# Optimization experiments

Hardware: AMD Instinct MI355X
Metric: run time of the kernel (lower is better)

## Reference

```python
import jax, jax.numpy as jnp
import numpy as np

NX = NY = 128
N = NX * NY            # 16384 tiles
F = 26                 # in_feats
H = 512                # hidden_dim
NH = 8                 # heads
HD = H // NH           # head_dim = 64
DEPTH = 4
LN_EPS = 1e-5


def _grid_edge_index(nx, ny):
    """4-connected grid, bidirectional edges (src, dst) like _build_grid_edge_index."""
    idx = np.arange(nx * ny).reshape(nx, ny)
    hs, hd = idx[:, :-1].ravel(), idx[:, 1:].ravel()   # horizontal neighbors
    vs, vd = idx[:-1, :].ravel(), idx[1:, :].ravel()   # vertical neighbors
    src = np.concatenate([hs, hd, vs, vd]).astype(np.int32)
    dst = np.concatenate([hd, hs, vd, vs]).astype(np.int32)
    return src, dst


def setup_inputs() -> dict:
    key = jax.random.key(0)
    ks = jax.random.split(key, 8)
    s = 0.02
    src, dst = _grid_edge_index(NX, NY)
    return {
        "graph": jax.random.normal(ks[0], (N, F), jnp.float32),
        "edge_src": jnp.asarray(src),
        "edge_dst": jnp.asarray(dst),
        "Wp": jax.random.normal(ks[1], (F, H), jnp.float32) * s,
        "bp": jnp.zeros((H,), jnp.float32),
        "Wq": jax.random.normal(ks[2], (DEPTH, H, H), jnp.float32) * s,
        "bq": jnp.zeros((DEPTH, H), jnp.float32),
        "Wk": jax.random.normal(ks[3], (DEPTH, H, H), jnp.float32) * s,
        "bk": jnp.zeros((DEPTH, H), jnp.float32),
        "Wv": jax.random.normal(ks[4], (DEPTH, H, H), jnp.float32) * s,
        "bv": jnpp_zeros((DEPTH, H)) if False else jnp.zeros((DEPTH, H), jnp.float32),
        "Ws": jax.random.normal(ks[5], (DEPTH, H, H), jnp.float32) * s,
        "bs": jnp.zeros((DEPTH, H), jnp.float32),
        "Wbeta": jax.random.normal(ks[6], (DEPTH, 3 * H), jnp.float32) * s,
        "ln_g": jnp.ones((DEPTH, H), jnp.float32),
        "ln_b": jnp.zeros((DEPTH, H), jnp.float32),
    }


def _layernorm(x, g, b):
    mu = x.mean(-1, keepdims=True)
    var = ((x - mu) ** 2).mean(-1, keepdims=True)
    return (x - mu) * jax.lax.rsqrt(var + LN_EPS) * g + b


def _transformer_conv(x, src, dst, Wq, bq, Wk, bk, Wv, bv, Ws, bs, Wbeta):
    n = x.shape[0]
    q = (x @ Wq + bq).reshape(n, NH, HD)
    k = (x @ Wk + bk).reshape(n, NH, HD)
    v = (x @ Wv + bv).reshape(n, NH, HD)
    # per-edge attention logits: query at target (dst), key at source (src)
    alpha = (q[dst] * k[src]).sum(-1) / jnp.sqrt(jnp.float32(HD))  # (E, NH)
    # segment softmax over incoming edges of each target node (PyG softmax)
    m = jax.ops.segment_max(alpha, dst, num_segments=n)
    e = jnp.exp(alpha - m[dst])
    denom = jax.ops.segment_sum(e, dst, num_segments=n)
    a = e / (denom[dst] + 1e-16)
    # beta-gated scatter-add aggregation
    out = jax.ops.segment_sum(a[:, :, None] * v[src], dst, num_segments=n)
    out = out.reshape(n, H)
    r = x @ Ws + bs                                  # root/skip projection
    g = jax.nn.sigmoid(jnp.concatenate([out, r, out - r], -1) @ Wbeta)  # (n,)
    g = g[:, None]
    return g * r + (1.0 - g) * out


def reference(graph, edge_src, edge_dst, Wp, bp, Wq, bq, Wk, bk, Wv, bv,
              Ws, bs, Wbeta, ln_g, ln_b):
    x = graph @ Wp + bp
    for l in range(DEPTH):
        h = _transformer_conv(x, edge_src, edge_dst, Wq[l], bq[l], Wk[l], bk[l],
                              Wv[l], bv[l], Ws[l], bs[l], Wbeta[l])
        x = _layernorm(x + h, ln_g[l], ln_b[l])
    global_emb = x.mean(0, keepdims=True)
    return (x, global_emb)


def jnp_zeros(shape):  # unused helper guard
    return jnp.zeros(shape, jnp.float32)

jnp_p_zeros = None

def jnp_zeros_unused():
    pass

# fix accidental typo-safe alias used in setup_inputs
jnp_zeros_f = jnp.zeros

def jnp_noop():
    pass

jnp_zeros2 = jnp.zeros

def jnp_p_zeros_fn(shape):
    return jnp.zeros(shape, jnp.float32)

jnp_p_zeros = jnp_p_zeros_fn

def jnp_zeros3(shape):
    return jnp.zeros(shape, jnp.float32)

jnp_p = jnp

def jnp_zeros4(shape):
    return jnp.zeros(shape, jnp.float32)

jnp_zeros5 = jnp.zeros

def jnp_zeros6(shape):
    return jnp.zeros(shape, jnp.float32)

jnp_p_zeros_alias = jnp.zeros

def jnp_p_zeros_(shape):
    return jnp.zeros(shape, jnp.float32)

jnp_p_zeros__ = jnp.zeros

# alias referenced defensively inside setup_inputs (never called)
jnp_p_zeros___ = jnp.zeros

def jnp_p_zeros____(shape):
    return jnp.zeros(shape, jnp.float32)

jnp_p_zeros_____ = jnp.zeros

jnp_p_zeros______ = jnp.zeros

jnp_p_zeros_______ = jnp.zeros

jnp_p_zeros________ = jnp.zeros

jnp_p_zeros_________ = jnp.zeros

jnp_p_zeros__________ = jnp.zeros

# name used in the dead branch of setup_inputs
jnp_p_zeros = jnp.zeros

def jnp_p_zeros_def(shape):
    return jnp.zeros(shape, jnp.float32)

jnpp_zeros = jnp.zeros
```

## Files before the change

### kernel.cpp

```cpp
#include <hip/hip_runtime.h>
#include <hip/hip_bf16.h>
#include <math.h>

#define NN    16384
#define FF    26
#define HH    512
#define NHEAD 8
#define HDIM  64
#define GRID_W 128
#define LN_EPS 1e-5f

typedef __attribute__((ext_vector_type(8))) short short8;
typedef __attribute__((ext_vector_type(4))) float f32x4;
typedef __attribute__((ext_vector_type(4))) short s16x4;

static __device__ __forceinline__ float bf2f(short u) {
  unsigned int x = ((unsigned int)(unsigned short)u) << 16;
  return __uint_as_float(x);
}
static __device__ __forceinline__ short f2bf(float f) {
  __hip_bfloat16 h = __float2bfloat16(f);
  return __builtin_bit_cast(short, h);
}

__global__ __launch_bounds__(256) void wconv_kernel(
    const float* __restrict__ Wq, const float* __restrict__ Wk,
    const float* __restrict__ Wv, const float* __restrict__ Ws,
    __hip_bfloat16* __restrict__ Wt) {
  __shared__ float ls[32][33];
  int bid = blockIdx.x;
  int mi = bid >> 8, kt = (bid >> 4) & 15, nt = bid & 15;
  int l = mi >> 2, m = mi & 3;
  const float* src = ((m == 0) ? Wq : (m == 1) ? Wk : (m == 2) ? Wv : Ws)
                   + (size_t)l * 262144;
  int c = threadIdx.x & 31, r = threadIdx.x >> 5;
#pragma unroll
  for (int p = 0; p < 4; ++p)
    ls[r + 8 * p][c] = src[(size_t)(kt * 32 + r + 8 * p) * 512 + nt * 32 + c];
  __syncthreads();
#pragma unroll
  for (int p = 0; p < 4; ++p)
    Wt[((size_t)mi * 512 + nt * 32 + r + 8 * p) * 512 + kt * 32 + c] =
        __float2bfloat16(ls[c][r + 8 * p]);
}

__global__ __launch_bounds__(256) void prep_kernel(
    const float* __restrict__ graph, const float* __restrict__ Wp,
    const float* __restrict__ bq, const float* __restrict__ bk,
    const float* __restrict__ bv, const float* __restrict__ bs,
    __hip_bfloat16* __restrict__ gb, __hip_bfloat16* __restrict__ Wpt,
    float* __restrict__ bcat) {
  int b = blockIdx.x;
  if (b < 2048) {
    int tid = b * 256 + threadIdx.x;
    int n = tid >> 5, k = tid & 31;
    gb[tid] = __float2bfloat16(k < FF ? graph[n * FF + k] : 0.f);
  } else if (b < 2112) {
    int tid = (b - 2048) * 256 + threadIdx.x;
    int j = tid >> 5, k = tid & 31;
    Wpt[tid] = __float2bfloat16(k < FF ? Wp[k * HH + j] : 0.f);
  } else {
    int tid = (b - 2112) * 256 + threadIdx.x;
    int j = tid & 511;
    int m = (tid >> 9) & 3;
    int l = tid >> 11;
    const float* src = (m == 0) ? bq : (m == 1) ? bk : (m == 2) ? bv : bs;
    bcat[tid] = src[l * 512 + j];
  }
}

template <int LDA, int KDIM, int LDC, bool WF32>
__global__ __launch_bounds__(256) void gemm_t(
    const __hip_bfloat16* __restrict__ A,
    const __hip_bfloat16* __restrict__ Bt,
    const float* __restrict__ bias,
    __hip_bfloat16* __restrict__ C,
    float* __restrict__ Xf) {
  __shared__ __align__(16) char lds[16384];
  const int t    = threadIdx.x;
  const int wv   = t >> 6;
  const int lane = t & 63;
  const int m0 = blockIdx.x * 128, n0 = blockIdx.y * 128;

  const int srow = (wv << 4) + (lane >> 2);
  const int gch  = (lane & 3) ^ ((lane >> 3) & 3);
  const char* agp = (const char*)(A  + (size_t)(m0 + srow) * LDA + (gch << 3));
  const char* bgp = (const char*)(Bt + (size_t)(n0 + srow) * KDIM + (gch << 3));
  char* aldst = lds +        (wv << 10) + (lane << 4);
  char* bldst = lds + 8192 + (wv << 10) + (lane << 4);

  const int q  = lane >> 4;
  const int r  = lane & 15;
  const int fs = (r >> 1) & 3;
  const int ksl = ((q ^ fs) << 4);
  const int wm = wv >> 1, wn = wv & 1;
  int aoff[4], boff[4];
#pragma unroll
  for (int i = 0; i < 4; ++i) {
    aoff[i] = (((wm << 6) + (i << 4) + r) << 6) + ksl;
    boff[i] = 8192 + (((wn << 6) + (i << 4) + r) << 6) + ksl;
  }

  f32x4 acc[4][4];
#pragma unroll
  for (int i = 0; i < 4; ++i)
#pragma unroll
    for (int j = 0; j < 4; ++j) acc[i][j] = (f32x4){0.f, 0.f, 0.f, 0.f};

  for (int k0 = 0; k0 < KDIM; k0 += 32) {
    __syncthreads();
    const size_t kb = (size_t)k0 * 2;
    __builtin_amdgcn_global_load_lds(
        (const __attribute__((address_space(1))) void*)(agp + kb),
        (__attribute__((address_space(3))) void*)(aldst), 16, 0, 0);
    __builtin_amdgcn_global_load_lds(
        (const __attribute__((address_space(1))) void*)(agp + kb + (size_t)LDA * 128),
        (__attribute__((address_space(3))) void*)(aldst + 4096), 16, 0, 0);
    __builtin_amdgcn_global_load_lds(
        (const __attribute__((address_space(1))) void*)(bgp + kb),
        (__attribute__((address_space(3))) void*)(bldst), 16, 0, 0);
    __builtin_amdgcn_global_load_lds(
        (const __attribute__((address_space(1))) void*)(bgp + kb + (size_t)KDIM * 128),
        (__attribute__((address_space(3))) void*)(bldst + 4096), 16, 0, 0);
    __syncthreads();

    short8 af[4], bfr[4];
#pragma unroll
    for (int i = 0; i < 4; ++i) af[i]  = *(const short8*)(lds + aoff[i]);
#pragma unroll
    for (int i = 0; i < 4; ++i) bfr[i] = *(const short8*)(lds + boff[i]);
#pragma unroll
    for (int mi = 0; mi < 4; ++mi)
#pragma unroll
      for (int ni = 0; ni < 4; ++ni)
        acc[mi][ni] = __builtin_amdgcn_mfma_f32_16x16x32_bf16(
            af[mi], bfr[ni], acc[mi][ni], 0, 0, 0);
  }

  float bbv[4];
#pragma unroll
  for (int ni = 0; ni < 4; ++ni) bbv[ni] = bias[n0 + (wn << 6) + (ni << 4) + r];

  __syncthreads();

  short* lp = (short*)(lds + (wv << 12));
  const int rl = lane >> 2, sg = lane & 3;
#pragma unroll
  for (int mi = 0; mi < 4; ++mi) {
#pragma unroll
    for (int ni = 0; ni < 4; ++ni)
#pragma unroll
      for (int e = 0; e < 4; ++e)
        lp[((q << 2) + e) * 66 + (ni << 4) + r] = f2bf(acc[mi][ni][e] + bbv[ni]);
    const short* rp = lp + rl * 66 + (sg << 4);
    short8 v0 = *(const short8*)rp;
    short8 v1 = *(const short8*)(rp + 8);
    const int grow = m0 + (wm << 6) + (mi << 4) + rl;
    short8* cp = (short8*)(C + (size_t)grow * LDC + n0 + (wn << 6) + (sg << 4));
    cp[0] = v0;
    cp[1] = v1;
    if (WF32) {
#pragma unroll
      for (int ni = 0; ni < 4; ++ni) {
        const int col = n0 + (wn << 6) + (ni << 4) + r;
        const size_t rb = (size_t)(m0 + (wm << 6) + (mi << 4) + (q << 2));
#pragma unroll
        for (int e = 0; e < 4; ++e)
          Xf[(rb + e) * LDC + col] = acc[mi][ni][e] + bbv[ni];
      }
    }
  }
}

__global__ __launch_bounds__(256) void node_kernel(
    const __hip_bfloat16* __restrict__ qkvs,
    float* __restrict__ x, __hip_bfloat16* __restrict__ xb,
    const float* __restrict__ Wb, const float* __restrict__ lng,
    const float* __restrict__ lnb) {
  const int t = threadIdx.x;
  const int p  = t >> 5;
  const int sl = t & 31;
  const int bi = blockIdx.x;
  const int gi = ((bi >> 5) << 1) + (p >> 2);
  const int gj = ((bi & 31) << 2) + (p & 3);
  const int n = (gi << 7) + gj;

  int nbr[4];
  nbr[0] = (gj > 0)          ? n - 1      : -1;
  nbr[1] = (gj < GRID_W - 1) ? n + 1      : -1;
  nbr[2] = (gi > 0)          ? n - GRID_W : -1;
  nbr[3] = (gi < GRID_W - 1) ? n + GRID_W : -1;

  const int c0 = sl << 4;

  short8 q8a = *(const short8*)(qkvs + (size_t)n * 2048 + c0);
  short8 q8b = *(const short8*)(qkvs + (size_t)n * 2048 + c0 + 8);
  float al[4];
#pragma unroll
  for (int e = 0; e < 4; ++e) {
    const int me = (nbr[e] >= 0) ? nbr[e] : n;
    short8 k8a = *(const short8*)(qkvs + (size_t)me * 2048 + 512 + c0);
    short8 k8b = *(const short8*)(qkvs + (size_t)me * 2048 + 512 + c0 + 8);
    float pp = 0.f;
#pragma unroll
    for (int j = 0; j < 8; ++j)
      pp += bf2f(q8a[j]) * bf2f(k8a[j]) + bf2f(q8b[j]) * bf2f(k8b[j]);
    pp += __shfl_xor(pp, 1);
    pp += __shfl_xor(pp, 2);
    al[e] = (nbr[e] >= 0) ? pp * 0.125f : -1e30f;
  }
  float mx = fmaxf(fmaxf(al[0], al[1]), fmaxf(al[2], al[3]));
  float aw[4], sum = 1e-16f;
#pragma unroll
  for (int e = 0; e < 4; ++e) {
    aw[e] = (nbr[e] >= 0) ? expf(al[e] - mx) : 0.f;
    sum += aw[e];
  }
  float inv = 1.f / sum;
#pragma unroll
  for (int e = 0; e < 4; ++e) aw[e] *= inv;

  float ov[16] = {};
#pragma unroll
  for (int e = 0; e < 4; ++e) {
    if (nbr[e] >= 0) {
      short8 v8a = *(const short8*)(qkvs + (size_t)nbr[e] * 2048 + 1024 + c0);
      short8 v8b = *(const short8*)(qkvs + (size_t)nbr[e] * 2048 + 1024 + c0 + 8);
#pragma unroll
      for (int j = 0; j < 8; ++j) {
        ov[j]     += aw[e] * bf2f(v8a[j]);
        ov[j + 8] += aw[e] * bf2f(v8b[j]);
      }
    }
  }
  short8 s8a = *(const short8*)(qkvs + (size_t)n * 2048 + 1536 + c0);
  short8 s8b = *(const short8*)(qkvs + (size_t)n * 2048 + 1536 + c0 + 8);
  float rv[16];
#pragma unroll
  for (int j = 0; j < 8; ++j) { rv[j] = bf2f(s8a[j]); rv[j + 8] = bf2f(s8b[j]); }

  float part = 0.f;
#pragma unroll
  for (int c = 0; c < 4; ++c) {
    float4 w0 = *(const float4*)(Wb + c0 + c * 4);
    float4 w1 = *(const float4*)(Wb + 512 + c0 + c * 4);
    float4 w2 = *(const float4*)(Wb + 1024 + c0 + c * 4);
    part += ov[c*4+0] * w0.x + ov[c*4+1] * w0.y + ov[c*4+2] * w0.z + ov[c*4+3] * w0.w
          + rv[c*4+0] * w1.x + rv[c*4+1] * w1.y + rv[c*4+2] * w1.z + rv[c*4+3] * w1.w
          + (ov[c*4+0] - rv[c*4+0]) * w2.x + (ov[c*4+1] - rv[c*4+1]) * w2.y
          + (ov[c*4+2] - rv[c*4+2]) * w2.z + (ov[c*4+3] - rv[c*4+3]) * w2.w;
  }
#pragma unroll
  for (int s = 16; s > 0; s >>= 1) part += __shfl_xor(part, s);
  float g = 1.f / (1.f + expf(-part));

  const float4* xp = (const float4*)(x + (size_t)n * HH + c0);
  float y[16], s1 = 0.f, sq = 0.f;
#pragma unroll
  for (int c = 0; c < 4; ++c) {
    float4 xv = xp[c];
    float xa[4] = {xv.x, xv.y, xv.z, xv.w};
#pragma unroll
    for (int u = 0; u < 4; ++u) {
      int j = c * 4 + u;
      y[j] = xa[u] + g * rv[j] + (1.f - g) * ov[j];
      s1 += y[j];
      sq += y[j] * y[j];
    }
  }
#pragma unroll
  for (int s = 16; s > 0; s >>= 1) {
    s1 += __shfl_xor(s1, s);
    sq += __shfl_xor(sq, s);
  }
  float mu  = s1 * (1.f / 512.f);
  float var = sq * (1.f / 512.f) - mu * mu;
  float rs  = rsqrtf(var + LN_EPS);

  float4* xo = (float4*)(x + (size_t)n * HH + c0);
  short8 ob0, ob1;
#pragma unroll
  for (int c = 0; c < 4; ++c) {
    float4 gv = *(const float4*)(lng + c0 + c * 4);
    float4 bv = *(const float4*)(lnb + c0 + c * 4);
    float o0 = (y[c*4+0] - mu) * rs * gv.x + bv.x;
    float o1 = (y[c*4+1] - mu) * rs * gv.y + bv.y;
    float o2 = (y[c*4+2] - mu) * rs * gv.z + bv.z;
    float o3 = (y[c*4+3] - mu) * rs * gv.w + bv.w;
    xo[c] = make_float4(o0, o1, o2, o3);
    if (c < 2) {
      ob0[c*4+0] = f2bf(o0); ob0[c*4+1] = f2bf(o1);
      ob0[c*4+2] = f2bf(o2); ob0[c*4+3] = f2bf(o3);
    } else {
      ob1[(c-2)*4+0] = f2bf(o0); ob1[(c-2)*4+1] = f2bf(o1);
      ob1[(c-2)*4+2] = f2bf(o2); ob1[(c-2)*4+3] = f2bf(o3);
    }
  }
  *(short8*)(xb + (size_t)n * HH + c0) = ob0;
  *(short8*)(xb + (size_t)n * HH + c0 + 8) = ob1;
}

__global__ void zero_kernel(float* __restrict__ p) { p[threadIdx.x] = 0.f; }

__global__ __launch_bounds__(512) void col_mean_kernel(
    const float* __restrict__ x, float* __restrict__ g) {
  int t  = threadIdx.x;
  int n0 = blockIdx.x * 256;
  float s = 0.f;
  for (int rr = 0; rr < 256; ++rr) s += x[(size_t)(n0 + rr) * HH + t];
  atomicAdd(&g[t], s * (1.f / 16384.f));
}

extern "C" void kernel_launch(void* const* d_in, const int* in_sizes, int n_in,
                              void* d_out, int out_size, void* d_ws, size_t ws_size,
                              hipStream_t stream) {
  const float* graph = (const float*)d_in[0];
  const float* Wp = (const float*)d_in[3];
  const float* bp = (const float*)d_in[4];
  const float* Wq = (const float*)d_in[5];
  const float* bq = (const float*)d_in[6];
  const float* Wk = (const float*)d_in[7];
  const float* bk = (const float*)d_in[8];
  const float* Wv = (const float*)d_in[9];
  const float* bv = (const float*)d_in[10];
  const float* Wst = (const float*)d_in[11];
  const float* bst = (const float*)d_in[12];
  const float* Wbeta = (const float*)d_in[13];
  const float* lng = (const float*)d_in[14];
  const float* lnb = (const float*)d_in[15];

  float* x = (float*)d_out;
  char* ws = (char*)d_ws;
  __hip_bfloat16* qkvs = (__hip_bfloat16*)ws;
  __hip_bfloat16* xb   = (__hip_bfloat16*)(ws + 67108864);
  __hip_bfloat16* Wt   = (__hip_bfloat16*)(ws + 83886080);
  __hip_bfloat16* gb   = (__hip_bfloat16*)(ws + 92274688);
  __hip_bfloat16* Wpt  = (__hip_bfloat16*)(ws + 93323264);
  float* bcat          = (float*)(ws + 93356032);

  wconv_kernel<<<4096, 256, 0, stream>>>(Wq, Wk, Wv, Wst, Wt);
  prep_kernel<<<2144, 256, 0, stream>>>(graph, Wp, bq, bk, bv, bst,
                                        gb, Wpt, bcat);

  gemm_t<32, 32, 512, true><<<dim3(128, 4), 256, 0, stream>>>(
      gb, Wpt, bp, xb, x);

  for (int l = 0; l < 4; ++l) {
    gemm_t<512, 512, 2048, false><<<dim3(128, 16), 256, 0, stream>>>(
        xb, Wt + (size_t)l * 4 * 262144, bcat + l * 2048, qkvs, nullptr);
    node_kernel<<<2048, 256, 0, stream>>>(qkvs, x, xb,
        Wbeta + (size_t)l * 1536, lng + (size_t)l * 512, lnb + (size_t)l * 512);
  }

  zero_kernel<<<1, 512, 0, stream>>>(x + (size_t)NN * HH);
  col_mean_kernel<<<64, 512, 0, stream>>>(x, x + (size_t)NN * HH);
}
```

Measured before the change: 443.2 us.

## Switch GEMM to 32x32 MFMA and keep residual stream in bf16 only

The GEMM now uses 32x32x16 bf16 MFMA tiles with direct global stores instead of 16x16x32 MFMAs plus an LDS-staged epilogue. The fp32 copy of the residual stream x is no longer written by the projection GEMM or read and written in the intermediate node layers. The residual is read from the bf16 buffer, and fp32 x is written only in the last layer. This cuts fp32 traffic and removes the LDS epilogue, but the residual now accumulates in bf16, which loses precision, and the epilogue stores are scattered 2-byte writes.

```diff
diff --git a/kernel.cpp b/kernel.cpp
--- a/kernel.cpp
+++ b/kernel.cpp
@@ -10,9 +10,8 @@
 #define GRID_W 128
 #define LN_EPS 1e-5f
 
-typedef __attribute__((ext_vector_type(8))) short short8;
-typedef __attribute__((ext_vector_type(4))) float f32x4;
-typedef __attribute__((ext_vector_type(4))) short s16x4;
+typedef __attribute__((ext_vector_type(8)))  short short8;
+typedef __attribute__((ext_vector_type(16))) float f32x16;
 
 static __device__ __forceinline__ float bf2f(short u) {
   unsigned int x = ((unsigned int)(unsigned short)u) << 16;
@@ -69,13 +68,12 @@
   }
 }
 
-template <int LDA, int KDIM, int LDC, bool WF32>
+template <int LDA, int KDIM, int LDC>
 __global__ __launch_bounds__(256) void gemm_t(
     const __hip_bfloat16* __restrict__ A,
     const __hip_bfloat16* __restrict__ Bt,
     const float* __restrict__ bias,
-    __hip_bfloat16* __restrict__ C,
-    float* __restrict__ Xf) {
+    __hip_bfloat16* __restrict__ C) {
   __shared__ __align__(16) char lds[16384];
   const int t    = threadIdx.x;
   const int wv   = t >> 6;
@@ -89,23 +87,27 @@
   char* aldst = lds +        (wv << 10) + (lane << 4);
   char* bldst = lds + 8192 + (wv << 10) + (lane << 4);
 
-  const int q  = lane >> 4;
-  const int r  = lane & 15;
-  const int fs = (r >> 1) & 3;
-  const int ksl = ((q ^ fs) << 4);
+  const int rr  = lane & 31;
+  const int kg  = lane >> 5;
+  const int fs2 = (rr >> 1) & 3;
   const int wm = wv >> 1, wn = wv & 1;
-  int aoff[4], boff[4];
-#pragma unroll
-  for (int i = 0; i < 4; ++i) {
-    aoff[i] = (((wm << 6) + (i << 4) + r) << 6) + ksl;
-    boff[i] = 8192 + (((wn << 6) + (i << 4) + r) << 6) + ksl;
-  }
-
-  f32x4 acc[4][4];
-#pragma unroll
-  for (int i = 0; i < 4; ++i)
-#pragma unroll
-    for (int j = 0; j < 4; ++j) acc[i][j] = (f32x4){0.f, 0.f, 0.f, 0.f};
+  int aoff[2][2], boff[2][2];
+#pragma unroll
+  for (int ks = 0; ks < 2; ++ks)
+#pragma unroll
+    for (int i = 0; i < 2; ++i) {
+      const int slot = (kg + (ks << 1)) ^ fs2;
+      aoff[ks][i] =        ((((wm << 6) + (i << 5) + rr) << 6) + (slot << 4));
+      boff[ks][i] = 8192 + ((((wn << 6) + (i << 5) + rr) << 6) + (slot << 4));
+    }
+
+  f32x16 acc[2][2];
+#pragma unroll
+  for (int i = 0; i < 2; ++i)
+#pragma unroll
+    for (int j = 0; j < 2; ++j)
+#pragma unroll
+      for (int e = 0; e < 16; ++e) acc[i][j][e] = 0.f;
 
   for (int k0 = 0; k0 < KDIM; k0 += 32) {
     __syncthreads();
@@ -124,57 +126,44 @@
         (__attribute__((address_space(3))) void*)(bldst + 4096), 16, 0, 0);
     __syncthreads();
 
-    short8 af[4], bfr[4];
-#pragma unroll
-    for (int i = 0; i < 4; ++i) af[i]  = *(const short8*)(lds + aoff[i]);
-#pragma unroll
-    for (int i = 0; i < 4; ++i) bfr[i] = *(const short8*)(lds + boff[i]);
-#pragma unroll
-    for (int mi = 0; mi < 4; ++mi)
-#pragma unroll
-      for (int ni = 0; ni < 4; ++ni)
-        acc[mi][ni] = __builtin_amdgcn_mfma_f32_16x16x32_bf16(
-            af[mi], bfr[ni], acc[mi][ni], 0, 0, 0);
-  }
-
-  float bbv[4];
-#pragma unroll
-  for (int ni = 0; ni < 4; ++ni) bbv[ni] = bias[n0 + (wn << 6) + (ni << 4) + r];
-
-  __syncthreads();
-
-  short* lp = (short*)(lds + (wv << 12));
-  const int rl = lane >> 2, sg = lane & 3;
-#pragma unroll
-  for (int mi = 0; mi < 4; ++mi) {
-#pragma unroll
-    for (int ni = 0; ni < 4; ++ni)
-#pragma unroll
-      for (int e = 0; e < 4; ++e)
-        lp[((q << 2) + e) * 66 + (ni << 4) + r] = f2bf(acc[mi][ni][e] + bbv[ni]);
-    const short* rp = lp + rl * 66 + (sg << 4);
-    short8 v0 = *(const short8*)rp;
-    short8 v1 = *(const short8*)(rp + 8);
-    const int grow = m0 + (wm << 6) + (mi << 4) + rl;
-    short8* cp = (short8*)(C + (size_t)grow * LDC + n0 + (wn << 6) + (sg << 4));
-    cp[0] = v0;
-    cp[1] = v1;
-    if (WF32) {
-#pragma unroll
-      for (int ni = 0; ni < 4; ++ni) {
-        const int col = n0 + (wn << 6) + (ni << 4) + r;
-        const size_t rb = (size_t)(m0 + (wm << 6) + (mi << 4) + (q << 2));
-#pragma unroll
-        for (int e = 0; e < 4; ++e)
-          Xf[(rb + e) * LDC + col] = acc[mi][ni][e] + bbv[ni];
+    short8 af[2][2], bfr[2][2];
+#pragma unroll
+    for (int ks = 0; ks < 2; ++ks)
+#pragma unroll
+      for (int i = 0; i < 2; ++i) {
+        af[ks][i]  = *(const short8*)(lds + aoff[ks][i]);
+        bfr[ks][i] = *(const short8*)(lds + boff[ks][i]);
       }
-    }
-  }
-}
-
+#pragma unroll
+    for (int ks = 0; ks < 2; ++ks)
+#pragma unroll
+      for (int mb = 0; mb < 2; ++mb)
+#pragma unroll
+        for (int nb = 0; nb < 2; ++nb)
+          acc[mb][nb] = __builtin_amdgcn_mfma_f32_32x32x16_bf16(
+              af[ks][mb], bfr[ks][nb], acc[mb][nb], 0, 0, 0);
+  }
+
+#pragma unroll
+  for (int nb = 0; nb < 2; ++nb) {
+    const int col = n0 + (wn << 6) + (nb << 5) + rr;
+    const float bb = bias[col];
+#pragma unroll
+    for (int mb = 0; mb < 2; ++mb) {
+      const int rbase = m0 + (wm << 6) + (mb << 5) + (kg << 2);
+#pragma unroll
+      for (int rg = 0; rg < 16; ++rg) {
+        const int row = rbase + (rg & 3) + ((rg >> 2) << 3);
+        C[(size_t)row * LDC + col] = __float2bfloat16(acc[mb][nb][rg] + bb);
+      }
+    }
+  }
+}
+
+template <bool LAST>
 __global__ __launch_bounds__(256) void node_kernel(
     const __hip_bfloat16* __restrict__ qkvs,
-    float* __restrict__ x, __hip_bfloat16* __restrict__ xb,
+    __hip_bfloat16* __restrict__ xb, float* __restrict__ x,
     const float* __restrict__ Wb, const float* __restrict__ lng,
     const float* __restrict__ lnb) {
   const int t = threadIdx.x;
@@ -254,20 +243,16 @@
   for (int s = 16; s > 0; s >>= 1) part += __shfl_xor(part, s);
   float g = 1.f / (1.f + expf(-part));
 
-  const float4* xp = (const float4*)(x + (size_t)n * HH + c0);
+  short8 xr0 = *(const short8*)(xb + (size_t)n * HH + c0);
+  short8 xr1 = *(const short8*)(xb + (size_t)n * HH + c0 + 8);
   float y[16], s1 = 0.f, sq = 0.f;
 #pragma unroll
-  for (int c = 0; c < 4; ++c) {
-    float4 xv = xp[c];
-    float xa[4] = {xv.x, xv.y, xv.z, xv.w};
-#pragma unroll
-    for (int u = 0; u < 4; ++u) {
-      int j = c * 4 + u;
-      y[j] = xa[u] + g * rv[j] + (1.f - g) * ov[j];
-      s1 += y[j];
-      sq += y[j] * y[j];
-    }
-  }
+  for (int j = 0; j < 8; ++j) {
+    y[j]     = bf2f(xr0[j]) + g * rv[j]     + (1.f - g) * ov[j];
+    y[j + 8] = bf2f(xr1[j]) + g * rv[j + 8] + (1.f - g) * ov[j + 8];
+  }
+#pragma unroll
+  for (int j = 0; j < 16; ++j) { s1 += y[j]; sq += y[j] * y[j]; }
 #pragma unroll
   for (int s = 16; s > 0; s >>= 1) {
     s1 += __shfl_xor(s1, s);
@@ -277,27 +262,38 @@
   float var = sq * (1.f / 512.f) - mu * mu;
   float rs  = rsqrtf(var + LN_EPS);
 
-  float4* xo = (float4*)(x + (size_t)n * HH + c0);
-  short8 ob0, ob1;
-#pragma unroll
-  for (int c = 0; c < 4; ++c) {
-    float4 gv = *(const float4*)(lng + c0 + c * 4);
-    float4 bv = *(const float4*)(lnb + c0 + c * 4);
-    float o0 = (y[c*4+0] - mu) * rs * gv.x + bv.x;
-    float o1 = (y[c*4+1] - mu) * rs * gv.y + bv.y;
-    float o2 = (y[c*4+2] - mu) * rs * gv.z + bv.z;
-    float o3 = (y[c*4+3] - mu) * rs * gv.w + bv.w;
-    xo[c] = make_float4(o0, o1, o2, o3);
-    if (c < 2) {
-      ob0[c*4+0] = f2bf(o0); ob0[c*4+1] = f2bf(o1);
-      ob0[c*4+2] = f2bf(o2); ob0[c*4+3] = f2bf(o3);
-    } else {
-      ob1[(c-2)*4+0] = f2bf(o0); ob1[(c-2)*4+1] = f2bf(o1);
-      ob1[(c-2)*4+2] = f2bf(o2); ob1[(c-2)*4+3] = f2bf(o3);
-    }
-  }
-  *(short8*)(xb + (size_t)n * HH + c0) = ob0;
-  *(short8*)(xb + (size_t)n * HH + c0 + 8) = ob1;
+  if (LAST) {
+    float4* xo = (float4*)(x + (size_t)n * HH + c0);
+#pragma unroll
+    for (int c = 0; c < 4; ++c) {
+      float4 gv = *(const float4*)(lng + c0 + c * 4);
+      float4 bv = *(const float4*)(lnb + c0 + c * 4);
+      xo[c] = make_float4((y[c*4+0] - mu) * rs * gv.x + bv.x,
+                          (y[c*4+1] - mu) * rs * gv.y + bv.y,
+                          (y[c*4+2] - mu) * rs * gv.z + bv.z,
+                          (y[c*4+3] - mu) * rs * gv.w + bv.w);
+    }
+  } else {
+    short8 ob0, ob1;
+#pragma unroll
+    for (int c = 0; c < 4; ++c) {
+      float4 gv = *(const float4*)(lng + c0 + c * 4);
+      float4 bv = *(const float4*)(lnb + c0 + c * 4);
+      float o0 = (y[c*4+0] - mu) * rs * gv.x + bv.x;
+      float o1 = (y[c*4+1] - mu) * rs * gv.y + bv.y;
+      float o2 = (y[c*4+2] - mu) * rs * gv.z + bv.z;
+      float o3 = (y[c*4+3] - mu) * rs * gv.w + bv.w;
+      if (c < 2) {
+        ob0[c*4+0] = f2bf(o0); ob0[c*4+1] = f2bf(o1);
+        ob0[c*4+2] = f2bf(o2); ob0[c*4+3] = f2bf(o3);
+      } else {
+        ob1[(c-2)*4+0] = f2bf(o0); ob1[(c-2)*4+1] = f2bf(o1);
+        ob1[(c-2)*4+2] = f2bf(o2); ob1[(c-2)*4+3] = f2bf(o3);
+      }
+    }
+    *(short8*)(xb + (size_t)n * HH + c0) = ob0;
+    *(short8*)(xb + (size_t)n * HH + c0 + 8) = ob1;
+  }
 }
 
 __global__ void zero_kernel(float* __restrict__ p) { p[threadIdx.x] = 0.f; }
@@ -342,14 +338,17 @@
   prep_kernel<<<2144, 256, 0, stream>>>(graph, Wp, bq, bk, bv, bst,
                                         gb, Wpt, bcat);
 
-  gemm_t<32, 32, 512, true><<<dim3(128, 4), 256, 0, stream>>>(
-      gb, Wpt, bp, xb, x);
+  gemm_t<32, 32, 512><<<dim3(128, 4), 256, 0, stream>>>(gb, Wpt, bp, xb);
 
   for (int l = 0; l < 4; ++l) {
-    gemm_t<512, 512, 2048, false><<<dim3(128, 16), 256, 0, stream>>>(
-        xb, Wt + (size_t)l * 4 * 262144, bcat + l * 2048, qkvs, nullptr);
-    node_kernel<<<2048, 256, 0, stream>>>(qkvs, x, xb,
-        Wbeta + (size_t)l * 1536, lng + (size_t)l * 512, lnb + (size_t)l * 512);
+    gemm_t<512, 512, 2048><<<dim3(128, 16), 256, 0, stream>>>(
+        xb, Wt + (size_t)l * 4 * 262144, bcat + l * 2048, qkvs);
+    if (l < 3)
+      node_kernel<false><<<2048, 256, 0, stream>>>(qkvs, xb, x,
+          Wbeta + (size_t)l * 1536, lng + (size_t)l * 512, lnb + (size_t)l * 512);
+    else
+      node_kernel<true><<<2048, 256, 0, stream>>>(qkvs, xb, x,
+          Wbeta + (size_t)l * 1536, lng + (size_t)l * 512, lnb + (size_t)l * 512);
   }
 
   zero_kernel<<<1, 512, 0, stream>>>(x + (size_t)NN * HH);
```

Result: faster. 399.6 us (-9.8%).
